# Performance work log

Hardware: AMD Instinct MI355X
Metric: run time of the kernel (lower is better)

## Reference

```python
import jax, jax.numpy as jnp
import numpy as np

B, C, N_ELEM = 16, 256, 8192
N_FILT, N_DIL = 2, 256


def setup_inputs() -> dict:
    key = jax.random.key(0)
    kx, kw = jax.random.split(key)
    x = jax.random.normal(kx, (B, C, N_ELEM), dtype=jnp.float32)
    # xavier_uniform on a (n_out, n_in, n_filt) tensor: fan_in = fan_out = C * N_FILT
    fan = C * N_FILT
    bound = float(np.sqrt(6.0 / (fan + fan)))
    weight = jax.random.uniform(kw, (C, C, N_FILT), minval=-bound, maxval=bound, dtype=jnp.float32)
    return {"x": x, "weight": weight, "n_dil": N_DIL}


def reference(x, weight, n_dil):
    # x: (B, C_in, N); weight: (C_out, C_in, n_filt); requires C_out == C_in.
    n_out, n_in, n_filt = weight.shape
    filter_size = (n_filt - 1) * n_dil + 1
    n_steps = x.shape[2] - filter_size

    # The torch loop computes, for i in [0, n_steps):
    #   x[:, :, i+1] = sum_{c,k} weight[o, c, k] * x_read[:, c, i + k*n_dil]
    # where the k=0 tap reads the UPDATED x (written at step i-1) and all
    # k>=1 taps read the ORIGINAL x (those positions are written at later
    # steps, and torch evaluates the conv before the in-place write).
    # => affine recurrence: s[i+1] = W0 @ s[i] + c[i], s[0] = x[:, :, 0].

    # c[t] = sum_{k>=1} W_k @ x_orig[:, :, t + k*n_dil]  -> (n_steps, B, C_out)
    c = jnp.zeros((n_steps, x.shape[0], n_out), dtype=x.dtype)
    for k in range(1, n_filt):
        xk = x[:, :, k * n_dil: k * n_dil + n_steps]  # (B, C_in, n_steps)
        c = c + jnp.einsum('oc,bct->tbo', weight[:, :, k], xk)

    W0T = weight[:, :, 0].T  # (C_in, C_out)

    def step(state, ct):
        # state: (B, C); ct: (B, C)
        new = state @ W0T + ct
        return new, new

    _, ys = jax.lax.scan(step, x[:, :, 0], c)  # ys: (n_steps, B, C)
    x_out = x.at[:, :, 1:1 + n_steps].set(jnp.transpose(ys, (1, 2, 0)))
    return x_out
```

## Files before the change

### kernel.cpp

```cpp
#include <hip/hip_runtime.h>
#include <stdint.h>


constexpr int BATCH  = 16;
constexpr int CH     = 256;
constexpr int NEL    = 8192;
constexpr int NDIL   = 256;
constexpr int TSTEPS = NEL - (NDIL + 1);
constexpr int LCH    = 16;
constexpr int NCH    = (TSTEPS + LCH - 1) / LCH;
constexpr int OUT_L  = 32;
constexpr int WARM   = 20;
constexpr int NCH2   = (TSTEPS + OUT_L - 1) / OUT_L;
constexpr int TPB    = 256;
constexpr int YPAD   = 260;
constexpr int A2PAD  = 264;
constexpr int TTILES = (TSTEPS + 127) / 128;
constexpr int YROW   = 264;

constexpr size_t OFF_AF    = 0;
constexpr size_t OFF_P1    = OFF_AF    + 256 * 1024;
constexpr size_t OFF_P2    = OFF_P1    + 256 * 1024;
constexpr size_t OFF_AB16  = OFF_P2    + 256 * 1024;
constexpr size_t OFF_W1B   = OFF_AB16  + 128 * 1024;
constexpr size_t OFF_E     = OFF_W1B   + 128 * 1024;
constexpr size_t OFF_INIT  = OFF_E     + (size_t)NCH * BATCH * CH * 4;
constexpr size_t OFF_AFRAG = OFF_INIT  + (size_t)(NCH + 1) * BATCH * CH * 4;
constexpr size_t OFF_W1FR  = OFF_AFRAG + 128 * 1024;
constexpr size_t OFF_CBUF  = OFF_W1FR  + 128 * 1024;
constexpr size_t CBUF_BYTES = (size_t)(NCH * LCH) * BATCH * CH * 2;
constexpr size_t OFF_YBUF  = OFF_CBUF + CBUF_BYTES;
constexpr size_t WS_NEED   = OFF_YBUF + CBUF_BYTES;

typedef __attribute__((ext_vector_type(8))) short bf16x8;
typedef __attribute__((ext_vector_type(4))) float f32x4;

__device__ __forceinline__ float bfu(uint32_t hibits) { return __uint_as_float(hibits); }
__device__ __forceinline__ float bf2f(uint16_t b) { return __uint_as_float(((uint32_t)b) << 16); }
__device__ __forceinline__ uint16_t f2bf(float f) {
  uint32_t u = __float_as_uint(f);
  uint32_t r = u + 0x7fffu + ((u >> 16) & 1u);
  return (uint16_t)(r >> 16);
}

__global__ void k_prep(const float* __restrict__ w, float* __restrict__ Af,
                       uint16_t* __restrict__ Ab, uint16_t* __restrict__ W1b,
                       uint16_t* __restrict__ Afrag, uint16_t* __restrict__ W1f) {
  int o = blockIdx.x, c = threadIdx.x;
  const float2 wv = *(const float2*)&w[(size_t)(o * CH + c) * 2];
  Af[c * CH + o]  = wv.x;
  Ab[c * CH + o]  = f2bf(wv.x);
  W1b[c * CH + o] = f2bf(wv.y);
  if (Afrag) {
    int kb = c >> 5, g = (c >> 3) & 3, ii = c & 7;
    int nt = o >> 4, mm = o & 15;
    size_t idx = (((size_t)(kb * 16 + nt) * 64) + (g * 16 + mm)) * 8 + ii;
    Afrag[idx] = f2bf(wv.x);
    W1f[idx]   = f2bf(wv.y);
  }
}

__global__ void k_init0(const float* __restrict__ x, float* __restrict__ initbuf) {
  int b = blockIdx.x, c = threadIdx.x;
  initbuf[b * CH + c] = x[(size_t)(b * CH + c) * NEL];
}

__global__ __launch_bounds__(TPB) void k_sqmm(const float* __restrict__ in,
                                              float* __restrict__ outm) {
  __shared__ __align__(16) float row[CH];
  int r = blockIdx.x, o = threadIdx.x;
  row[o] = in[r * CH + o];
  __syncthreads();
  float acc = 0.f;
#pragma unroll 8
  for (int k = 0; k < CH; ++k) acc += row[k] * in[k * CH + o];
  outm[r * CH + o] = acc;
}

__global__ void k_edges(const float* __restrict__ x, float* __restrict__ out) {
  size_t base = (size_t)blockIdx.x * NEL;
  int t = threadIdx.x;
  out[base + (NEL - 256) + t] = x[base + (NEL - 256) + t];
  if (t == 0) out[base] = x[base];
}

__global__ __launch_bounds__(512, 4) void k_cgemm_m(const float* __restrict__ x,
                                                    const uint16_t* __restrict__ W1f,
                                                    uint16_t* __restrict__ cb) {
  __shared__ __align__(16) uint16_t Axs[64 * 64 * 8];
  int tid = threadIdx.x, bid = blockIdx.x;
  int b = bid / TTILES, tt = bid % TTILES;
  int t0 = tt * 128;
  int w = tid >> 6, l = tid & 63, lm = l & 15, g = l >> 4;
  const float* xb = x + (size_t)b * CH * NEL + (t0 + NDIL);

  bf16x8 bv[8][2];
#pragma unroll
  for (int kb = 0; kb < 8; ++kb)
#pragma unroll
    for (int p = 0; p < 2; ++p)
      bv[kb][p] =
          *(const bf16x8*)&W1f[(((size_t)(kb * 16 + w * 2 + p) * 64) + l) * 8];

  int tA = w * 16 + lm;
#pragma unroll
  for (int kb = 0; kb < 8; ++kb) {
    float v[8];
#pragma unroll
    for (int i = 0; i < 8; ++i)
      v[i] = xb[(size_t)(kb * 32 + g * 8 + i) * NEL + tA];
    uint4 pk;
    pk.x = (uint32_t)f2bf(v[0]) | ((uint32_t)f2bf(v[1]) << 16);
    pk.y = (uint32_t)f2bf(v[2]) | ((uint32_t)f2bf(v[3]) << 16);
    pk.z = (uint32_t)f2bf(v[4]) | ((uint32_t)f2bf(v[5]) << 16);
    pk.w = (uint32_t)f2bf(v[6]) | ((uint32_t)f2bf(v[7]) << 16);
    *(uint4*)&Axs[((w * 8 + kb) * 64 + l) * 8] = pk;
  }
  __syncthreads();

#pragma unroll 1
  for (int mt = 0; mt < 8; ++mt) {
    f32x4 acc0 = (f32x4)0.f, acc1 = (f32x4)0.f;
#pragma unroll
    for (int kb = 0; kb < 8; ++kb) {
      bf16x8 av = *(const bf16x8*)&Axs[((mt * 8 + kb) * 64 + l) * 8];
      acc0 = __builtin_amdgcn_mfma_f32_16x16x32_bf16(av, bv[kb][0], acc0, 0, 0, 0);
      acc1 = __builtin_amdgcn_mfma_f32_16x16x32_bf16(av, bv[kb][1], acc1, 0, 0, 0);
    }
#pragma unroll
    for (int r = 0; r < 4; ++r) {
      int t2 = t0 + mt * 16 + g * 4 + r;
      if (t2 < TSTEPS) {
        size_t base = (size_t)t2 * (BATCH * CH) + b * CH;
        cb[base + (w * 2 + 0) * 16 + lm] = f2bf(acc0[r]);
        cb[base + (w * 2 + 1) * 16 + lm] = f2bf(acc1[r]);
      }
    }
  }
}

__device__ __forceinline__ void scan2_step(
    int t, bool pref, bool doout, const uint16_t* Yr, uint16_t* Yw,
    const uint16_t* __restrict__ cb, uint16_t* __restrict__ yb,
    const bf16x8 af[8][4], ushort* cc, int w, int lm, int g, int tid) {
  bf16x8 yv[8];
#pragma unroll
  for (int kb = 0; kb < 8; ++kb)
    yv[kb] = *(const bf16x8*)&Yr[lm * YROW + kb * 32 + g * 8];
  f32x4 acc[4];
#pragma unroll
  for (int ntl = 0; ntl < 4; ++ntl)
#pragma unroll
    for (int r = 0; r < 4; ++r)
      acc[ntl][r] = bfu(((uint32_t)cc[ntl * 4 + r]) << 16);
  if (pref) {
    size_t cbase = (size_t)(t + 2) * (BATCH * CH);
#pragma unroll
    for (int ntl = 0; ntl < 4; ++ntl)
#pragma unroll
      for (int r = 0; r < 4; ++r)
        cc[ntl * 4 + r] = cb[cbase + (g * 4 + r) * CH + (w * 4 + ntl) * 16 + lm];
  }
#pragma unroll
  for (int ntl = 0; ntl < 4; ++ntl) {
#pragma unroll
    for (int kb = 0; kb < 8; ++kb)
      acc[ntl] = __builtin_amdgcn_mfma_f32_16x16x32_bf16(yv[kb], af[kb][ntl], acc[ntl], 0, 0, 0);
  }
  uint16_t hbv[16];
#pragma unroll
  for (int ntl = 0; ntl < 4; ++ntl)
#pragma unroll
    for (int r = 0; r < 4; ++r) {
      float v = acc[ntl][r];
      int bb = g * 4 + r, o = (w * 4 + ntl) * 16 + lm;
      uint16_t hb = f2bf(v);
      hbv[ntl * 4 + r] = hb;
      Yw[bb * YROW + o] = hb;
    }
  if (doout) {
    uint4 p0, p1;
    p0.x = (uint32_t)hbv[0] | ((uint32_t)hbv[1] << 16);
    p0.y = (uint32_t)hbv[2] | ((uint32_t)hbv[3] << 16);
    p0.z = (uint32_t)hbv[4] | ((uint32_t)hbv[5] << 16);
    p0.w = (uint32_t)hbv[6] | ((uint32_t)hbv[7] << 16);
    p1.x = (uint32_t)hbv[8] | ((uint32_t)hbv[9] << 16);
    p1.y = (uint32_t)hbv[10] | ((uint32_t)hbv[11] << 16);
    p1.z = (uint32_t)hbv[12] | ((uint32_t)hbv[13] << 16);
    p1.w = (uint32_t)hbv[14] | ((uint32_t)hbv[15] << 16);
    uint4* dst = (uint4*)&yb[(size_t)t * 4096 + tid * 16];
    dst[0] = p0;
    dst[1] = p1;
  }
  asm volatile("s_waitcnt lgkmcnt(0)" ::: "memory");
  __builtin_amdgcn_sched_barrier(0);
  __builtin_amdgcn_s_barrier();
  __builtin_amdgcn_sched_barrier(0);
}

__global__ __launch_bounds__(TPB, 2) void k_scan2(
    const uint16_t* __restrict__ Afrag, const uint16_t* __restrict__ cb,
    uint16_t* __restrict__ yb, const float* __restrict__ x) {
  __shared__ __align__(16) uint16_t Y[2][16 * YROW];
  int tid = threadIdx.x;
  int j = blockIdx.x;
  int w = tid >> 6, l = tid & 63;
  int lm = l & 15, g = l >> 4;

  bf16x8 af[8][4];
#pragma unroll
  for (int kb = 0; kb < 8; ++kb)
#pragma unroll
    for (int ntl = 0; ntl < 4; ++ntl) {
      int nt = w * 4 + ntl;
      af[kb][ntl] = *(const bf16x8*)&Afrag[(((size_t)(kb * 16 + nt) * 64) + l) * 8];
    }

  int tstart   = (j == 0) ? 0 : OUT_L * j - WARM;
  int outstart = OUT_L * j;
  int tend     = min(OUT_L * (j + 1), TSTEPS);

  if (j == 0) {
    int b = tid >> 4, o0 = (tid & 15) * 16;
#pragma unroll
    for (int q = 0; q < 16; ++q)
      Y[0][b * YROW + o0 + q] = f2bf(x[(size_t)(b * CH + o0 + q) * NEL]);
  } else {
    for (int q = tid; q < 16 * YROW; q += TPB) Y[0][q] = 0;
  }

  ushort c0[16], c1[16];
  {
#pragma unroll
    for (int ntl = 0; ntl < 4; ++ntl)
#pragma unroll
      for (int r = 0; r < 4; ++r) {
        size_t off = (size_t)(g * 4 + r) * CH + (w * 4 + ntl) * 16 + lm;
        c0[ntl * 4 + r] = cb[(size_t)tstart * (BATCH * CH) + off];
        c1[ntl * 4 + r] = cb[(size_t)(tstart + 1) * (BATCH * CH) + off];
      }
  }
  __syncthreads();

#pragma unroll 1
  for (int ii = 0; ii < OUT_L + WARM + 2; ii += 2) {
    int t = tstart + ii;
    if (t >= tend) break;
    scan2_step(t, t + 2 < tend, t >= outstart, Y[0], Y[1], cb, yb,
               af, c0, w, lm, g, tid);
    if (t + 1 >= tend) break;
    scan2_step(t + 1, t + 3 < tend, t + 1 >= outstart, Y[1], Y[0], cb, yb,
               af, c1, w, lm, g, tid);
  }
}

__global__ __launch_bounds__(TPB) void k_yout(const uint16_t* __restrict__ yb,
                                              float* __restrict__ out) {
  __shared__ __align__(16) uint16_t t2[256 * 72];
  int bid = blockIdx.x;
  int tb = bid >> 4, sub = bid & 15;
  int G = sub >> 2, wS = sub & 3;
  int t0 = tb * 64;
  int tid = threadIdx.x;
  {
    int tl = tid >> 2, part = tid & 3;
    const uint16_t* src =
        &yb[(size_t)(t0 + tl) * 4096 + (wS * 64 + G * 16) * 16 + part * 64];
#pragma unroll
    for (int i = 0; i < 8; ++i) {
      uint4 vv = *(const uint4*)&src[i * 8];
      uint32_t uu[4] = {vv.x, vv.y, vv.z, vv.w};
      int colb = part * 64 + i * 8;
#pragma unroll
      for (int e = 0; e < 4; ++e) {
        t2[(colb + 2 * e) * 72 + tl]     = (uint16_t)(uu[e] & 0xffffu);
        t2[(colb + 2 * e + 1) * 72 + tl] = (uint16_t)(uu[e] >> 16);
      }
    }
  }
  __syncthreads();
  {
    int b = G * 4 + (tid >> 6);
    int o = wS * 64 + (tid & 63);
    int col = (o & 15) * 16 + ((o >> 4) & 3) * 4 + (b & 3);
    float* dst = &out[(size_t)(b * CH + o) * NEL + 1 + t0];
    bool full = (t0 + 63 < TSTEPS);
#pragma unroll
    for (int k4 = 0; k4 < 4; ++k4) {
      uint4 v0 = *(const uint4*)&t2[col * 72 + k4 * 16];
      uint4 v1 = *(const uint4*)&t2[col * 72 + k4 * 16 + 8];
      uint32_t uu[8] = {v0.x, v0.y, v0.z, v0.w, v1.x, v1.y, v1.z, v1.w};
      float f[16];
#pragma unroll
      for (int e = 0; e < 8; ++e) {
        f[2 * e]     = bfu(uu[e] << 16);
        f[2 * e + 1] = bfu(uu[e] & 0xffff0000u);
      }
      if (full) {
#pragma unroll
        for (int m = 0; m < 4; ++m)
          *(float4*)&dst[k4 * 16 + m * 4] =
              make_float4(f[4 * m], f[4 * m + 1], f[4 * m + 2], f[4 * m + 3]);
      } else {
#pragma unroll
        for (int e = 0; e < 16; ++e)
          if (t0 + k4 * 16 + e < TSTEPS) dst[k4 * 16 + e] = f[e];
      }
    }
  }
}

__global__ __launch_bounds__(TPB) void k_cgemm_v(const float* __restrict__ x,
                                                 const uint16_t* __restrict__ W1b,
                                                 float* __restrict__ out) {
  __shared__ __align__(16) uint16_t w1[CH * 128];
  __shared__ __align__(16) float xs[32][128];
  int tid = threadIdx.x;
  int bid = blockIdx.x;
  int b = bid / (TTILES * 2);
  int rem = bid % (TTILES * 2);
  int ttile = rem >> 1, otile = rem & 1;
  int t0 = ttile * 128, o0 = otile * 128;
  int tx = tid & 15, ty = tid >> 4;
  int o8 = o0 + tx * 8;
  int tb = t0 + ty * 8;
  {
    uint4* dst = (uint4*)w1;
    for (int q = tid; q < CH * 128 / 8; q += TPB) {
      int row = q >> 4, seg = q & 15;
      dst[q] = *(const uint4*)&W1b[row * CH + o0 + seg * 8];
    }
  }
  float acc[8][8];
#pragma unroll
  for (int i = 0; i < 8; ++i)
#pragma unroll
    for (int j = 0; j < 8; ++j) acc[i][j] = 0.f;
  for (int c0 = 0; c0 < CH; c0 += 32) {
    __syncthreads();
#pragma unroll
    for (int kk = 0; kk < 4; ++kk) {
      int q = tid + kk * TPB;
      int cc = q >> 5, tf = (q & 31) * 4;
      *(float4*)&xs[cc][tf] =
          *(const float4*)&x[(size_t)(b * CH + c0 + cc) * NEL + t0 + NDIL + tf];
    }
    __syncthreads();
#pragma unroll 4
    for (int cc = 0; cc < 32; ++cc) {
      float4 xa = *(const float4*)&xs[cc][ty * 8];
      float4 xb = *(const float4*)&xs[cc][ty * 8 + 4];
      float xv[8] = {xa.x, xa.y, xa.z, xa.w, xb.x, xb.y, xb.z, xb.w};
      uint4 wv = *(const uint4*)&w1[(c0 + cc) * 128 + tx * 8];
      float wf[8] = {bfu(wv.x << 16), bfu(wv.x & 0xffff0000u),
                     bfu(wv.y << 16), bfu(wv.y & 0xffff0000u),
                     bfu(wv.z << 16), bfu(wv.z & 0xffff0000u),
                     bfu(wv.w << 16), bfu(wv.w & 0xffff0000u)};
#pragma unroll
      for (int i = 0; i < 8; ++i)
#pragma unroll
        for (int j = 0; j < 8; ++j) acc[i][j] += xv[i] * wf[j];
    }
  }
#pragma unroll
  for (int j = 0; j < 8; ++j) {
    size_t base = (size_t)(b * CH + o8 + j) * NEL + tb + 1;
#pragma unroll
    for (int i = 0; i < 8; ++i)
      if (tb + i < TSTEPS) out[base + i] = acc[i][j];
  }
}

template <bool PH3>
__global__ __launch_bounds__(TPB) void k_scan(const uint16_t* __restrict__ Ab,
                                              const float* __restrict__ initbuf,
                                              float* __restrict__ Ebuf,
                                              float* __restrict__ out) {
  __shared__ __align__(16) uint16_t Al[CH * CH];
  __shared__ __align__(16) float yl[BATCH * YPAD];
  int tid = threadIdx.x;
  int j = blockIdx.x;
  {
    const uint4* src = (const uint4*)Ab;
    uint4* dst = (uint4*)Al;
    for (int q = tid; q < CH * CH / 8; q += TPB) dst[q] = src[q];
  }
  if constexpr (PH3) {
    for (int q = tid; q < BATCH * CH / 4; q += TPB) {
      int b = q >> 6, c4 = (q & 63) * 4;
      *(float4*)&yl[b * YPAD + c4] =
          *(const float4*)&initbuf[(size_t)j * BATCH * CH + b * CH + c4];
    }
  } else {
    for (int q = tid; q < BATCH * YPAD; q += TPB) yl[q] = 0.f;
  }
  __syncthreads();
  int o4 = (tid & 63) * 4;
  int b4 = (tid >> 6) * 4;
  int len = min(LCH, TSTEPS - j * LCH);
  float acc[4][4];
  for (int i = 0; i < len; ++i) {
    int t = j * LCH + i;
    float cv[4][4];
#pragma unroll
    for (int bb = 0; bb < 4; ++bb)
#pragma unroll
      for (int oo = 0; oo < 4; ++oo)
        cv[bb][oo] = out[(size_t)((b4 + bb) * CH + o4 + oo) * NEL + t + 1];
#pragma unroll
    for (int bb = 0; bb < 4; ++bb)
#pragma unroll
      for (int oo = 0; oo < 4; ++oo) acc[bb][oo] = 0.f;
#pragma unroll 2
    for (int c = 0; c < CH; c += 4) {
      float4 v0 = *(const float4*)&yl[(b4 + 0) * YPAD + c];
      float4 v1 = *(const float4*)&yl[(b4 + 1) * YPAD + c];
      float4 v2 = *(const float4*)&yl[(b4 + 2) * YPAD + c];
      float4 v3 = *(const float4*)&yl[(b4 + 3) * YPAD + c];
      float y0[4] = {v0.x, v0.y, v0.z, v0.w};
      float y1[4] = {v1.x, v1.y, v1.z, v1.w};
      float y2[4] = {v2.x, v2.y, v2.z, v2.w};
      float y3[4] = {v3.x, v3.y, v3.z, v3.w};
#pragma unroll
      for (int k = 0; k < 4; ++k) {
        uint2 au = *(const uint2*)&Al[(c + k) * CH + o4];
        float a[4] = {bfu(au.x << 16), bfu(au.x & 0xffff0000u),
                      bfu(au.y << 16), bfu(au.y & 0xffff0000u)};
#pragma unroll
        for (int oo = 0; oo < 4; ++oo) {
          acc[0][oo] += y0[k] * a[oo];
          acc[1][oo] += y1[k] * a[oo];
          acc[2][oo] += y2[k] * a[oo];
          acc[3][oo] += y3[k] * a[oo];
        }
      }
    }
#pragma unroll
    for (int bb = 0; bb < 4; ++bb)
#pragma unroll
      for (int oo = 0; oo < 4; ++oo) acc[bb][oo] += cv[bb][oo];
    __syncthreads();
#pragma unroll
    for (int bb = 0; bb < 4; ++bb)
      *(float4*)&yl[(b4 + bb) * YPAD + o4] =
          make_float4(acc[bb][0], acc[bb][1], acc[bb][2], acc[bb][3]);
    if constexpr (PH3) {
#pragma unroll
      for (int bb = 0; bb < 4; ++bb)
#pragma unroll
        for (int oo = 0; oo < 4; ++oo)
          out[(size_t)((b4 + bb) * CH + o4 + oo) * NEL + t + 1] = acc[bb][oo];
    }
    __syncthreads();
  }
  if constexpr (!PH3) {
#pragma unroll
    for (int bb = 0; bb < 4; ++bb)
#pragma unroll
      for (int oo = 0; oo < 4; ++oo)
        Ebuf[(size_t)j * BATCH * CH + (b4 + bb) * CH + o4 + oo] = acc[bb][oo];
  }
}

__global__ __launch_bounds__(TPB) void k_phase2(const float* __restrict__ ALf,
                                                const float* __restrict__ Ebuf,
                                                float* __restrict__ initbuf) {
  __shared__ __align__(16) uint16_t At[CH * A2PAD];
  __shared__ __align__(16) float st[CH];
  int b = blockIdx.x, tid = threadIdx.x;
  for (int q = tid; q < CH * CH; q += TPB) {
    int c = q >> 8, o = q & 255;
    At[o * A2PAD + c] = f2bf(ALf[q]);
  }
  st[tid] = initbuf[b * CH + tid];
  __syncthreads();
  for (int jj = 1; jj < NCH; ++jj) {
    float acc = Ebuf[(size_t)(jj - 1) * BATCH * CH + b * CH + tid];
#pragma unroll 4
    for (int c = 0; c < CH; c += 8) {
      uint4 au = *(const uint4*)&At[tid * A2PAD + c];
      float4 s0 = *(const float4*)&st[c];
      float4 s1 = *(const float4*)&st[c + 4];
      acc += bfu(au.x << 16) * s0.x + bfu(au.x & 0xffff0000u) * s0.y +
             bfu(au.y << 16) * s0.z + bfu(au.y & 0xffff0000u) * s0.w +
             bfu(au.z << 16) * s1.x + bfu(au.z & 0xffff0000u) * s1.y +
             bfu(au.w << 16) * s1.z + bfu(au.w & 0xffff0000u) * s1.w;
    }
    __syncthreads();
    st[tid] = acc;
    initbuf[(size_t)jj * BATCH * CH + b * CH + tid] = acc;
    __syncthreads();
  }
}

extern "C" void kernel_launch(void* const* d_in, const int* in_sizes, int n_in,
                              void* d_out, int out_size, void* d_ws, size_t ws_size,
                              hipStream_t stream) {
  const float* x = (const float*)d_in[0];
  const float* w = (const float*)d_in[1];
  float* out = (float*)d_out;
  char* ws = (char*)d_ws;

  float*    Af    = (float*)(ws + OFF_AF);
  float*    P1    = (float*)(ws + OFF_P1);
  float*    P2    = (float*)(ws + OFF_P2);
  uint16_t* Ab    = (uint16_t*)(ws + OFF_AB16);
  uint16_t* W1b   = (uint16_t*)(ws + OFF_W1B);
  float*    Ebuf  = (float*)(ws + OFF_E);
  float*    inb   = (float*)(ws + OFF_INIT);
  uint16_t* Afrag = (uint16_t*)(ws + OFF_AFRAG);
  uint16_t* W1f   = (uint16_t*)(ws + OFF_W1FR);
  uint16_t* cbuf  = (uint16_t*)(ws + OFF_CBUF);
  uint16_t* ybuf  = (uint16_t*)(ws + OFF_YBUF);

  const bool fast = ws_size >= WS_NEED;

  k_prep<<<CH, CH, 0, stream>>>(w, Af, Ab, W1b, fast ? Afrag : nullptr, W1f);
  k_edges<<<BATCH * CH, 256, 0, stream>>>(x, out);
  if (fast) {
    k_cgemm_m<<<BATCH * TTILES, 512, 0, stream>>>(x, W1f, cbuf);
    k_scan2<<<NCH2, TPB, 0, stream>>>(Afrag, cbuf, ybuf, x);
    k_yout<<<124 * 16, TPB, 0, stream>>>(ybuf, out);
  } else {
    k_init0<<<BATCH, CH, 0, stream>>>(x, inb);
    k_sqmm<<<CH, TPB, 0, stream>>>(Af, P1);
    k_sqmm<<<CH, TPB, 0, stream>>>(P1, P2);
    k_sqmm<<<CH, TPB, 0, stream>>>(P2, P1);
    k_sqmm<<<CH, TPB, 0, stream>>>(P1, P2);
    k_cgemm_v<<<BATCH * TTILES * 2, TPB, 0, stream>>>(x, W1b, out);
    k_scan<false><<<NCH - 1, TPB, 0, stream>>>(Ab, nullptr, Ebuf, out);
    k_phase2<<<BATCH, TPB, 0, stream>>>(P2, Ebuf, inb);
    k_scan<true><<<NCH, TPB, 0, stream>>>(Ab, inb, nullptr, out);
  }
}
```

Before: 203.9 us.

## Align y-output stores to 16-byte boundaries and batch x loads in cgemm

The output transpose kernel is shifted by one time step so each thread's float4 stores to out start on an aligned address. The first tile writes only elements 1..15 of its first group scalar-wise, and the partial-tile tail check is removed, which assumes the grid covers TSTEPS exactly up to the fixed edge region. The cgemm_m kernel now issues four k-blocks of x loads before converting and storing them, to raise memory-level parallelism. Its launch bound drops to 2 blocks per SM to allow more registers for this.

```diff
diff --git a/kernel.cpp b/kernel.cpp
--- a/kernel.cpp
+++ b/kernel.cpp
@@ -84,7 +84,7 @@
   if (t == 0) out[base] = x[base];
 }
 
-__global__ __launch_bounds__(512, 4) void k_cgemm_m(const float* __restrict__ x,
+__global__ __launch_bounds__(512, 2) void k_cgemm_m(const float* __restrict__ x,
                                                     const uint16_t* __restrict__ W1f,
                                                     uint16_t* __restrict__ cb) {
   __shared__ __align__(16) uint16_t Axs[64 * 64 * 8];
@@ -104,17 +104,22 @@
 
   int tA = w * 16 + lm;
 #pragma unroll
-  for (int kb = 0; kb < 8; ++kb) {
-    float v[8];
-#pragma unroll
-    for (int i = 0; i < 8; ++i)
-      v[i] = xb[(size_t)(kb * 32 + g * 8 + i) * NEL + tA];
-    uint4 pk;
-    pk.x = (uint32_t)f2bf(v[0]) | ((uint32_t)f2bf(v[1]) << 16);
-    pk.y = (uint32_t)f2bf(v[2]) | ((uint32_t)f2bf(v[3]) << 16);
-    pk.z = (uint32_t)f2bf(v[4]) | ((uint32_t)f2bf(v[5]) << 16);
-    pk.w = (uint32_t)f2bf(v[6]) | ((uint32_t)f2bf(v[7]) << 16);
-    *(uint4*)&Axs[((w * 8 + kb) * 64 + l) * 8] = pk;
+  for (int kq = 0; kq < 2; ++kq) {
+    float v[4][8];
+#pragma unroll
+    for (int k2 = 0; k2 < 4; ++k2)
+#pragma unroll
+      for (int i = 0; i < 8; ++i)
+        v[k2][i] = xb[(size_t)((kq * 4 + k2) * 32 + g * 8 + i) * NEL + tA];
+#pragma unroll
+    for (int k2 = 0; k2 < 4; ++k2) {
+      uint4 pk;
+      pk.x = (uint32_t)f2bf(v[k2][0]) | ((uint32_t)f2bf(v[k2][1]) << 16);
+      pk.y = (uint32_t)f2bf(v[k2][2]) | ((uint32_t)f2bf(v[k2][3]) << 16);
+      pk.z = (uint32_t)f2bf(v[k2][4]) | ((uint32_t)f2bf(v[k2][5]) << 16);
+      pk.w = (uint32_t)f2bf(v[k2][6]) | ((uint32_t)f2bf(v[k2][7]) << 16);
+      *(uint4*)&Axs[((w * 8 + kq * 4 + k2) * 64 + l) * 8] = pk;
+    }
   }
   __syncthreads();
 
@@ -264,17 +269,20 @@
   int tid = threadIdx.x;
   {
     int tl = tid >> 2, part = tid & 3;
-    const uint16_t* src =
-        &yb[(size_t)(t0 + tl) * 4096 + (wS * 64 + G * 16) * 16 + part * 64];
-#pragma unroll
-    for (int i = 0; i < 8; ++i) {
-      uint4 vv = *(const uint4*)&src[i * 8];
-      uint32_t uu[4] = {vv.x, vv.y, vv.z, vv.w};
-      int colb = part * 64 + i * 8;
-#pragma unroll
-      for (int e = 0; e < 4; ++e) {
-        t2[(colb + 2 * e) * 72 + tl]     = (uint16_t)(uu[e] & 0xffffu);
-        t2[(colb + 2 * e + 1) * 72 + tl] = (uint16_t)(uu[e] >> 16);
+    int ty = t0 + tl - 1;
+    if (ty >= 0) {
+      const uint16_t* src =
+          &yb[(size_t)ty * 4096 + (wS * 64 + G * 16) * 16 + part * 64];
+#pragma unroll
+      for (int i = 0; i < 8; ++i) {
+        uint4 vv = *(const uint4*)&src[i * 8];
+        uint32_t uu[4] = {vv.x, vv.y, vv.z, vv.w};
+        int colb = part * 64 + i * 8;
+#pragma unroll
+        for (int e = 0; e < 4; ++e) {
+          t2[(colb + 2 * e) * 72 + tl]     = (uint16_t)(uu[e] & 0xffffu);
+          t2[(colb + 2 * e + 1) * 72 + tl] = (uint16_t)(uu[e] >> 16);
+        }
       }
     }
   }
@@ -283,8 +291,7 @@
     int b = G * 4 + (tid >> 6);
     int o = wS * 64 + (tid & 63);
     int col = (o & 15) * 16 + ((o >> 4) & 3) * 4 + (b & 3);
-    float* dst = &out[(size_t)(b * CH + o) * NEL + 1 + t0];
-    bool full = (t0 + 63 < TSTEPS);
+    float* dst = &out[(size_t)(b * CH + o) * NEL + t0];
 #pragma unroll
     for (int k4 = 0; k4 < 4; ++k4) {
       uint4 v0 = *(const uint4*)&t2[col * 72 + k4 * 16];
@@ -296,15 +303,14 @@
         f[2 * e]     = bfu(uu[e] << 16);
         f[2 * e + 1] = bfu(uu[e] & 0xffff0000u);
       }
-      if (full) {
+      if (tb == 0 && k4 == 0) {
+#pragma unroll
+        for (int e = 1; e < 16; ++e) dst[e] = f[e];
+      } else {
 #pragma unroll
         for (int m = 0; m < 4; ++m)
           *(float4*)&dst[k4 * 16 + m * 4] =
               make_float4(f[4 * m], f[4 * m + 1], f[4 * m + 2], f[4 * m + 3]);
-      } else {
-#pragma unroll
-        for (int e = 0; e < 16; ++e)
-          if (t0 + k4 * 16 + e < TSTEPS) dst[k4 * 16 + e] = f[e];
       }
     }
   }
```

Result: faster. 192.2 us (-5.8%).
